# Kernel optimization log

Measured on AMD Instinct MI355X. Metric: run time of the kernel, lower is better.

The kernel has to match this reference:

```python
import jax, jax.numpy as jnp
import numpy as np

COF1 = 0.01
EPS = 1e-8  # matches F.cosine_similarity default eps


def setup_inputs() -> dict:
    key = jax.random.key(0)
    latent = jax.random.normal(key, (8192, 64), dtype=jnp.float32)
    return {"latent": latent}


def reference(latent):
    # rows whose elementwise sum is nonzero participate (as i and as j)
    mask = (jnp.sum(latent, axis=1) != 0).astype(latent.dtype)  # [N]
    # L2-normalize rows with eps clamp (cosine similarity denominator)
    norm = jnp.maximum(jnp.sqrt(jnp.sum(latent * latent, axis=1, keepdims=True)), EPS)
    ln = latent / norm  # [N, d]
    sim = ln @ ln.T  # [N, N] pairwise cosine similarities
    # sum over selected (i, j) pairs, minus 1 per selected row i (self-sim correction)
    total = jnp.einsum('i,ij,j->', mask, sim, mask) - jnp.sum(mask)
    n = latent.shape[0]
    return COF1 * total / (2.0 * n)
```

## Files before the change

### kernel.cpp

```cpp
#include <hip/hip_runtime.h>


#define EPSV 1e-8f
#define COF1 0.01f

constexpr int N_ROWS = 8192;
constexpr int DIM = 64;
constexpr int TPB = 256;
constexpr int WAVES_PER_BLOCK = TPB / 64;
constexpr int BLOCKS = 256;
constexpr int ROWS_PER_WAVE = N_ROWS / (BLOCKS * WAVES_PER_BLOCK);
constexpr int SLOT = 68;

__global__ __launch_bounds__(TPB, 2) void cl_partial(const float* __restrict__ latent,
                                                     float* __restrict__ ws) {
    const int wv   = threadIdx.x >> 6;
    const int lane = threadIdx.x & 63;
    const int g    = lane >> 4;
    const int c4   = lane & 15;
    const int row0 = (blockIdx.x * WAVES_PER_BLOCK + wv) * ROWS_PER_WAVE;

    const float4* lat4 = (const float4*)latent;

    float4 v = make_float4(0.f, 0.f, 0.f, 0.f);
    float cnt = 0.0f;

    #pragma unroll
    for (int b = 0; b < ROWS_PER_WAVE / 4; ++b) {
        const int row = row0 + b * 4 + g;
        float4 x = lat4[row * (DIM / 4) + c4];

        float s = x.x + x.y + x.z + x.w;
        float q = x.x * x.x + x.y * x.y + x.z * x.z + x.w * x.w;
        #pragma unroll
        for (int off = 8; off; off >>= 1) {
            s += __shfl_xor(s, off);
            q += __shfl_xor(q, off);
        }
        if (s != 0.0f) {
            float inv = 1.0f / fmaxf(sqrtf(q), EPSV);
            v.x += x.x * inv; v.y += x.y * inv;
            v.z += x.z * inv; v.w += x.w * inv;
            if (c4 == 0) cnt += 1.0f;
        }
    }

    #pragma unroll
    for (int off = 16; off <= 32; off <<= 1) {
        v.x += __shfl_xor(v.x, off); v.y += __shfl_xor(v.y, off);
        v.z += __shfl_xor(v.z, off); v.w += __shfl_xor(v.w, off);
        cnt += __shfl_xor(cnt, off);
    }

    __shared__ float4 sv4[WAVES_PER_BLOCK][16];
    __shared__ float  scnt[WAVES_PER_BLOCK];
    if (lane < 16) sv4[wv][c4] = v;
    if (lane == 0) scnt[wv] = cnt;
    __syncthreads();

    if (wv == 0 && lane < 16) {
        float4 a = sv4[0][c4];
        float4 b1 = sv4[1][c4], b2 = sv4[2][c4], b3 = sv4[3][c4];
        a.x += b1.x + b2.x + b3.x; a.y += b1.y + b2.y + b3.y;
        a.z += b1.z + b2.z + b3.z; a.w += b1.w + b2.w + b3.w;
        ((float4*)(ws + blockIdx.x * SLOT))[c4] = a;
        if (lane == 0)
            ws[blockIdx.x * SLOT + 64] = scnt[0] + scnt[1] + scnt[2] + scnt[3];
    }
}

__global__ __launch_bounds__(256) void cl_final(const float* __restrict__ ws,
                                                float* __restrict__ out) {
    const int wv   = threadIdx.x >> 6;
    const int lane = threadIdx.x & 63;

    const float* base = ws + (wv * 64) * SLOT;
    float acc = 0.0f, c = 0.0f;
    for (int b0 = 0; b0 < 64; b0 += 8) {
        float t[8], tc[8];
        #pragma unroll
        for (int j = 0; j < 8; ++j) {
            t[j]  = base[(b0 + j) * SLOT + lane];
            tc[j] = base[(b0 + j) * SLOT + 64];
        }
        #pragma unroll
        for (int j = 0; j < 8; ++j) { acc += t[j]; c += tc[j]; }
    }

    __shared__ float sv[WAVES_PER_BLOCK][64];
    __shared__ float scnt[WAVES_PER_BLOCK];
    sv[wv][lane] = acc;
    if (lane == 0) scnt[wv] = c;
    __syncthreads();

    if (wv == 0) {
        float a = sv[0][lane] + sv[1][lane] + sv[2][lane] + sv[3][lane];
        float d = a * a;
        #pragma unroll
        for (int off = 32; off; off >>= 1)
            d += __shfl_xor(d, off);
        if (lane == 0) {
            float ctot = scnt[0] + scnt[1] + scnt[2] + scnt[3];
            out[0] = COF1 * (d - ctot) / (2.0f * (float)N_ROWS);
        }
    }
}

extern "C" void kernel_launch(void* const* d_in, const int* in_sizes, int n_in,
                              void* d_out, int out_size, void* d_ws, size_t ws_size,
                              hipStream_t stream) {
    const float* latent = (const float*)d_in[0];
    float* out = (float*)d_out;
    float* ws = (float*)d_ws;

    cl_partial<<<BLOCKS, TPB, 0, stream>>>(latent, ws);
    cl_final<<<1, 256, 0, stream>>>(ws, out);
}
```

Before: 12.67 us.

## Fuse partial and final reduction kernels via release/acquire flags and block-0 spin

Merges the two-kernel reduction into one launch. Each block publishes its partial sums and then sets a per-block flag with a release atomic store. Block 0 spin-waits with acquire loads until all 256 flags are set, reduces the partials, and resets the flags for the next call. This removes the second kernel launch and the gap between kernels. It relies on every block being co-resident so block 0 cannot deadlock, and on the workspace being zeroed initially or never holding the magic value.

```diff
diff --git a/kernel.cpp b/kernel.cpp
--- a/kernel.cpp
+++ b/kernel.cpp
@@ -7,18 +7,21 @@
 constexpr int N_ROWS = 8192;
 constexpr int DIM = 64;
 constexpr int TPB = 256;
-constexpr int WAVES_PER_BLOCK = TPB / 64;
+constexpr int WPB = TPB / 64;
 constexpr int BLOCKS = 256;
-constexpr int ROWS_PER_WAVE = N_ROWS / (BLOCKS * WAVES_PER_BLOCK);
+constexpr int RPW = N_ROWS / (BLOCKS * WPB);
 constexpr int SLOT = 68;
+constexpr unsigned MAGIC = 0x5EEDF00Du;
 
-__global__ __launch_bounds__(TPB, 2) void cl_partial(const float* __restrict__ latent,
-                                                     float* __restrict__ ws) {
+__global__ __launch_bounds__(TPB, 2) void cl_fused(const float* __restrict__ latent,
+                                                   float* __restrict__ ws,
+                                                   unsigned* __restrict__ flags,
+                                                   float* __restrict__ out) {
     const int wv   = threadIdx.x >> 6;
     const int lane = threadIdx.x & 63;
     const int g    = lane >> 4;
     const int c4   = lane & 15;
-    const int row0 = (blockIdx.x * WAVES_PER_BLOCK + wv) * ROWS_PER_WAVE;
+    const int row0 = (blockIdx.x * WPB + wv) * RPW;
 
     const float4* lat4 = (const float4*)latent;
 
@@ -26,10 +29,9 @@
     float cnt = 0.0f;
 
     #pragma unroll
-    for (int b = 0; b < ROWS_PER_WAVE / 4; ++b) {
+    for (int b = 0; b < RPW / 4; ++b) {
         const int row = row0 + b * 4 + g;
         float4 x = lat4[row * (DIM / 4) + c4];
-
         float s = x.x + x.y + x.z + x.w;
         float q = x.x * x.x + x.y * x.y + x.z * x.z + x.w * x.w;
         #pragma unroll
@@ -44,7 +46,6 @@
             if (c4 == 0) cnt += 1.0f;
         }
     }
-
     #pragma unroll
     for (int off = 16; off <= 32; off <<= 1) {
         v.x += __shfl_xor(v.x, off); v.y += __shfl_xor(v.y, off);
@@ -52,8 +53,8 @@
         cnt += __shfl_xor(cnt, off);
     }
 
-    __shared__ float4 sv4[WAVES_PER_BLOCK][16];
-    __shared__ float  scnt[WAVES_PER_BLOCK];
+    __shared__ float4 sv4[WPB][16];
+    __shared__ float  scnt[WPB];
     if (lane < 16) sv4[wv][c4] = v;
     if (lane == 0) scnt[wv] = cnt;
     __syncthreads();
@@ -66,13 +67,19 @@
         ((float4*)(ws + blockIdx.x * SLOT))[c4] = a;
         if (lane == 0)
             ws[blockIdx.x * SLOT + 64] = scnt[0] + scnt[1] + scnt[2] + scnt[3];
+        __threadfence();
     }
-}
+    __syncthreads();
+    if (threadIdx.x == 0)
+        __hip_atomic_store(&flags[blockIdx.x], MAGIC,
+                           __ATOMIC_RELEASE, __HIP_MEMORY_SCOPE_AGENT);
 
-__global__ __launch_bounds__(256) void cl_final(const float* __restrict__ ws,
-                                                float* __restrict__ out) {
-    const int wv   = threadIdx.x >> 6;
-    const int lane = threadIdx.x & 63;
+    if (blockIdx.x != 0) return;
+
+    while (__hip_atomic_load(&flags[threadIdx.x],
+                             __ATOMIC_ACQUIRE, __HIP_MEMORY_SCOPE_AGENT) != MAGIC) {}
+    __syncthreads();
+    __threadfence();
 
     const float* base = ws + (wv * 64) * SLOT;
     float acc = 0.0f, c = 0.0f;
@@ -87,23 +94,25 @@
         for (int j = 0; j < 8; ++j) { acc += t[j]; c += tc[j]; }
     }
 
-    __shared__ float sv[WAVES_PER_BLOCK][64];
-    __shared__ float scnt[WAVES_PER_BLOCK];
-    sv[wv][lane] = acc;
-    if (lane == 0) scnt[wv] = c;
+    __shared__ float fv[WPB][64];
+    __shared__ float fc[WPB];
+    fv[wv][lane] = acc;
+    if (lane == 0) fc[wv] = c;
     __syncthreads();
 
     if (wv == 0) {
-        float a = sv[0][lane] + sv[1][lane] + sv[2][lane] + sv[3][lane];
+        float a = fv[0][lane] + fv[1][lane] + fv[2][lane] + fv[3][lane];
         float d = a * a;
         #pragma unroll
         for (int off = 32; off; off >>= 1)
             d += __shfl_xor(d, off);
         if (lane == 0) {
-            float ctot = scnt[0] + scnt[1] + scnt[2] + scnt[3];
+            float ctot = fc[0] + fc[1] + fc[2] + fc[3];
             out[0] = COF1 * (d - ctot) / (2.0f * (float)N_ROWS);
         }
     }
+    __syncthreads();
+    flags[threadIdx.x] = 0;
 }
 
 extern "C" void kernel_launch(void* const* d_in, const int* in_sizes, int n_in,
@@ -112,7 +121,7 @@
     const float* latent = (const float*)d_in[0];
     float* out = (float*)d_out;
     float* ws = (float*)d_ws;
+    unsigned* flags = (unsigned*)(ws + BLOCKS * SLOT);
 
-    cl_partial<<<BLOCKS, TPB, 0, stream>>>(latent, ws);
-    cl_final<<<1, 256, 0, stream>>>(ws, out);
+    cl_fused<<<BLOCKS, TPB, 0, stream>>>(latent, ws, flags, out);
 }
```

Result: slower. 18.03 us (+42.3%).
